# Optimization experiments

Hardware: AMD Instinct MI355X
Metric: run time of the kernel (lower is better)

The kernel has to match this reference:

```python
import jax, jax.numpy as jnp
import numpy as np
import math

B, L, D = 4, 2048, 512
H = 8
HD = D // H
K1 = 64  # local_window_size
K2 = 64  # global_window_size


def semi_local_mask(seq_len):
    # Faithful to create_semi_local_mask: anti-diagonal band + global prefix, ANDed with causal tril.
    i = jnp.arange(seq_len)[:, None]
    j = jnp.arange(seq_len)[None, :]
    band = (i + j >= seq_len - K1) & (i + j <= seq_len)
    glob = (j <= K2) & (j <= seq_len - i)
    causal = j <= i
    return (band | glob) & causal  # [L, L] bool


def setup_inputs() -> dict:
    key = jax.random.key(0)
    ks = jax.random.split(key, 8)
    def xavier(k, shape):
        fan_in, fan_out = shape[1], shape[0]
        lim = math.sqrt(6.0 / (fan_in + fan_out))
        return jax.random.uniform(k, shape, jnp.float32, -lim, lim)
    x = jax.random.normal(ks[0], (B, L, D), jnp.float32)
    w_qkv = xavier(ks[1], (3 * D, D)); b_qkv = jnp.zeros((3 * D,), jnp.float32)
    w_u = xavier(ks[2], (D, D));       b_u = jnp.zeros((D,), jnp.float32)
    w_out = xavier(ks[3], (D, D));     b_out = jnp.zeros((D,), jnp.float32)
    return {"x": x, "w_qkv": w_qkv, "b_qkv": b_qkv, "w_u": w_u, "b_u": b_u,
            "w_out": w_out, "b_out": b_out}


def reference(x, w_qkv, b_qkv, w_u, b_u, w_out, b_out):
    Bsz, Lq, Dm = x.shape
    qkv = (x @ w_qkv.T + b_qkv).reshape(Bsz, Lq, 3, H, HD)
    q, k, v = jnp.moveaxis(qkv, 2, 0)            # each [B, L, H, HD]
    q = jnp.transpose(q, (0, 2, 1, 3))           # [B, H, L, HD]
    k = jnp.transpose(k, (0, 2, 1, 3))
    v = jnp.transpose(v, (0, 2, 1, 3))
    u = x @ w_u.T + b_u                          # [B, L, D] (gate values)
    scale = 1.0 / math.sqrt(HD)
    scores = jnp.einsum('bhqd,bhkd->bhqk', q * scale, k)
    mask = semi_local_mask(Lq)                   # [L, L]
    scores = jnp.where(mask[None, None], scores, -jnp.inf)
    attn = jax.nn.softmax(scores, axis=-1)
    out = jnp.einsum('bhqk,bhkd->bhqd', attn, v)
    out = jnp.transpose(out, (0, 2, 1, 3)).reshape(Bsz, Lq, Dm)
    out = jax.nn.silu(out) * u
    return out @ w_out.T + b_out
```

## Files before the change

### kernel.cpp

```cpp
#include <hip/hip_runtime.h>
#include <hip/hip_bf16.h>

typedef __bf16 bf16x8 __attribute__((ext_vector_type(8)));
typedef float f32x4 __attribute__((ext_vector_type(4)));

#define B_ 4
#define L_ 2048
#define D_ 512
#define H_ 8

__device__ __forceinline__ void gl16(const __bf16* g, __bf16* l) {
  __builtin_amdgcn_global_load_lds(
      (const __attribute__((address_space(1))) void*)g,
      (__attribute__((address_space(3))) void*)l, 16, 0, 0);
}

__global__ __launch_bounds__(256) void cvt_pack(
    const float* __restrict__ x, const float* __restrict__ wq,
    const float* __restrict__ wu, const float* __restrict__ wo,
    const float* __restrict__ bq, const float* __restrict__ bu,
    __bf16* __restrict__ xb, __bf16* __restrict__ wcat,
    __bf16* __restrict__ wob, float* __restrict__ bcat)
{
  const int idx8 = blockIdx.x * 256 + threadIdx.x;
  const float* src; __bf16* dst; size_t so, dof;
  if (idx8 < 524288)      { src = x;  dst = xb;   so = (size_t)idx8 * 8;            dof = so; }
  else if (idx8 < 622592) { src = wq; dst = wcat; so = (size_t)(idx8 - 524288) * 8; dof = so; }
  else if (idx8 < 655360) { src = wu; dst = wcat; so = (size_t)(idx8 - 622592) * 8; dof = so + 786432; }
  else                    { src = wo; dst = wob;  so = (size_t)(idx8 - 655360) * 8; dof = so; }
  const float4 lo = *(const float4*)(src + so);
  const float4 hi = *(const float4*)(src + so + 4);
  bf16x8 r;
  r[0] = (__bf16)lo.x; r[1] = (__bf16)lo.y; r[2] = (__bf16)lo.z; r[3] = (__bf16)lo.w;
  r[4] = (__bf16)hi.x; r[5] = (__bf16)hi.y; r[6] = (__bf16)hi.z; r[7] = (__bf16)hi.w;
  *(bf16x8*)(dst + dof) = r;
  if (blockIdx.x == 0) {
#pragma unroll
    for (int e = 0; e < 8; ++e) {
      const int col = threadIdx.x * 8 + e;
      bcat[col] = (col < 1536) ? bq[col] : bu[col - 1536];
    }
  }
}

__global__ __launch_bounds__(512, 2) void gemm256(
    const __bf16* __restrict__ A, const __bf16* __restrict__ W,
    const float* __restrict__ bias, __bf16* __restrict__ C,
    int M, int N, int K)
{
  extern __shared__ char smem[];
  const int t = threadIdx.x;
  const int lane = t & 63;
  const int wave = t >> 6;
  const int wm = (wave >> 2) * 128;
  const int wn = (wave & 3) * 64;
  const int bm0 = blockIdx.x * 256;
  const int bn0 = blockIdx.y * 256;
  const int r = lane & 15, q = lane >> 4;
  const int nt = K >> 6;

  auto stage = [&](int kt, int p) {
#pragma unroll
    for (int j = 0; j < 4; ++j) {
      const int c = t + j * 512;
      const int row = c >> 3;
      const int cs = (c & 7) ^ (row & 7);
      gl16(A + (size_t)(bm0 + row) * K + kt * 64 + cs * 8,
           (__bf16*)(smem + p * 32768) + c * 8);
    }
#pragma unroll
    for (int j = 0; j < 4; ++j) {
      const int c = t + j * 512;
      const int row = c >> 3;
      const int cs = (c & 7) ^ (row & 7);
      gl16(W + (size_t)(bn0 + row) * K + kt * 64 + cs * 8,
           (__bf16*)(smem + 65536 + p * 32768) + c * 8);
    }
  };
  auto rdA = [&](int p, int mi, int ks) -> bf16x8 {
    const int row = wm + mi * 16 + r;
    const int byte = row * 128 + ((ks * 64 + q * 16) ^ ((row & 7) << 4));
    return *(const bf16x8*)(smem + p * 32768 + byte);
  };
  auto rdB = [&](int p, int ni, int ks) -> bf16x8 {
    const int row = wn + ni * 16 + r;
    const int byte = row * 128 + ((ks * 64 + q * 16) ^ ((row & 7) << 4));
    return *(const bf16x8*)(smem + 65536 + p * 32768 + byte);
  };

  f32x4 acc[8][4] = {};

  stage(0, 0);
  stage(1, 1);

  for (int kt = 0; kt < nt; ++kt) {
    const int p = kt & 1;
    if (kt < nt - 1) asm volatile("s_waitcnt vmcnt(8)" ::: "memory");
    else             asm volatile("s_waitcnt vmcnt(0)" ::: "memory");
    __builtin_amdgcn_sched_barrier(0);
    __builtin_amdgcn_s_barrier();
    __builtin_amdgcn_sched_barrier(0);

    bf16x8 a03[4][2], a47[4][2], b01[2][2], b23[2][2];
#pragma unroll
    for (int mi = 0; mi < 4; ++mi) { a03[mi][0] = rdA(p, mi, 0); a03[mi][1] = rdA(p, mi, 1); }
#pragma unroll
    for (int ni = 0; ni < 2; ++ni) { b01[ni][0] = rdB(p, ni, 0); b01[ni][1] = rdB(p, ni, 1); }
    __builtin_amdgcn_s_setprio(1);
#pragma unroll
    for (int mi = 0; mi < 4; ++mi)
#pragma unroll
      for (int ni = 0; ni < 2; ++ni) {
        acc[mi][ni] = __builtin_amdgcn_mfma_f32_16x16x32_bf16(a03[mi][0], b01[ni][0], acc[mi][ni], 0, 0, 0);
        acc[mi][ni] = __builtin_amdgcn_mfma_f32_16x16x32_bf16(a03[mi][1], b01[ni][1], acc[mi][ni], 0, 0, 0);
      }
    __builtin_amdgcn_s_setprio(0);
#pragma unroll
    for (int ni = 0; ni < 2; ++ni) { b23[ni][0] = rdB(p, ni + 2, 0); b23[ni][1] = rdB(p, ni + 2, 1); }
    __builtin_amdgcn_s_setprio(1);
#pragma unroll
    for (int mi = 0; mi < 4; ++mi)
#pragma unroll
      for (int ni = 0; ni < 2; ++ni) {
        acc[mi][ni + 2] = __builtin_amdgcn_mfma_f32_16x16x32_bf16(a03[mi][0], b23[ni][0], acc[mi][ni + 2], 0, 0, 0);
        acc[mi][ni + 2] = __builtin_amdgcn_mfma_f32_16x16x32_bf16(a03[mi][1], b23[ni][1], acc[mi][ni + 2], 0, 0, 0);
      }
    __builtin_amdgcn_s_setprio(0);
#pragma unroll
    for (int mi = 0; mi < 4; ++mi) { a47[mi][0] = rdA(p, mi + 4, 0); a47[mi][1] = rdA(p, mi + 4, 1); }
    __builtin_amdgcn_s_setprio(1);
#pragma unroll
    for (int mi = 0; mi < 4; ++mi)
#pragma unroll
      for (int ni = 0; ni < 2; ++ni) {
        acc[mi + 4][ni] = __builtin_amdgcn_mfma_f32_16x16x32_bf16(a47[mi][0], b01[ni][0], acc[mi + 4][ni], 0, 0, 0);
        acc[mi + 4][ni] = __builtin_amdgcn_mfma_f32_16x16x32_bf16(a47[mi][1], b01[ni][1], acc[mi + 4][ni], 0, 0, 0);
      }
    __builtin_amdgcn_s_setprio(0);
    asm volatile("s_waitcnt lgkmcnt(0)" ::: "memory");
    __builtin_amdgcn_sched_barrier(0);
    __builtin_amdgcn_s_barrier();
    __builtin_amdgcn_sched_barrier(0);
    if (kt + 2 < nt) stage(kt + 2, p);
    __builtin_amdgcn_s_setprio(1);
#pragma unroll
    for (int mi = 0; mi < 4; ++mi)
#pragma unroll
      for (int ni = 0; ni < 2; ++ni) {
        acc[mi + 4][ni + 2] = __builtin_amdgcn_mfma_f32_16x16x32_bf16(a47[mi][0], b23[ni][0], acc[mi + 4][ni + 2], 0, 0, 0);
        acc[mi + 4][ni + 2] = __builtin_amdgcn_mfma_f32_16x16x32_bf16(a47[mi][1], b23[ni][1], acc[mi + 4][ni + 2], 0, 0, 0);
      }
    __builtin_amdgcn_s_setprio(0);
  }

  const int cc = lane & 15, cq = lane >> 4;
#pragma unroll
  for (int mi = 0; mi < 8; ++mi) {
#pragma unroll
    for (int ni = 0; ni < 4; ++ni) {
      const int gcol = bn0 + wn + ni * 16 + cc;
      const float bv = bias[gcol];
#pragma unroll
      for (int rr = 0; rr < 4; ++rr) {
        const int grow = bm0 + wm + mi * 16 + cq * 4 + rr;
        C[(size_t)grow * N + gcol] = (__bf16)(acc[mi][ni][rr] + bv);
      }
    }
  }
}

template <typename TOUT>
__global__ __launch_bounds__(256) void gemm_async(
    const __bf16* __restrict__ A, const __bf16* __restrict__ W,
    const float* __restrict__ bias, TOUT* __restrict__ C,
    int M, int N, int K)
{
  __shared__ __bf16 lA[4096];
  __shared__ __bf16 lB[4096];
  const int t = threadIdx.x;
  const int lane = t & 63;
  const int wave = t >> 6;
  const int bm0 = blockIdx.x * 128;
  const int bn0 = blockIdx.y * 128;
  const int wm = (wave >> 1) * 64;
  const int wn = (wave & 1) * 64;

  f32x4 acc[4][4] = {};

  const __bf16* Ap0 = A + (size_t)(bm0 + (t >> 2)) * K + (t & 3) * 8;
  const __bf16* Bp0 = W + (size_t)(bn0 + (t >> 2)) * K + (t & 3) * 8;
  const size_t r64 = (size_t)64 * K;

  for (int k0 = 0; k0 < K; k0 += 32) {
    __syncthreads();
    gl16(Ap0 + k0,       lA + t * 8);
    gl16(Ap0 + r64 + k0, lA + (t + 256) * 8);
    gl16(Bp0 + k0,       lB + t * 8);
    gl16(Bp0 + r64 + k0, lB + (t + 256) * 8);
    __syncthreads();

    const int r = lane & 15, q = lane >> 4;
    bf16x8 af[4], bfr[4];
#pragma unroll
    for (int mi = 0; mi < 4; ++mi) af[mi] = ((const bf16x8*)lA)[(wm + mi * 16 + r) * 4 + q];
#pragma unroll
    for (int ni = 0; ni < 4; ++ni) bfr[ni] = ((const bf16x8*)lB)[(wn + ni * 16 + r) * 4 + q];
#pragma unroll
    for (int mi = 0; mi < 4; ++mi)
#pragma unroll
      for (int ni = 0; ni < 4; ++ni)
        acc[mi][ni] = __builtin_amdgcn_mfma_f32_16x16x32_bf16(af[mi], bfr[ni], acc[mi][ni], 0, 0, 0);
  }

  const int cc = lane & 15, cq = lane >> 4;
#pragma unroll
  for (int mi = 0; mi < 4; ++mi) {
#pragma unroll
    for (int ni = 0; ni < 4; ++ni) {
      const int gcol = bn0 + wn + ni * 16 + cc;
      const float bv = bias[gcol];
#pragma unroll
      for (int rr = 0; rr < 4; ++rr) {
        const int grow = bm0 + wm + mi * 16 + cq * 4 + rr;
        C[(size_t)grow * N + gcol] = (TOUT)(acc[mi][ni][rr] + bv);
      }
    }
  }
}

#define SP 72
#define QS 2048
__global__ __launch_bounds__(256) void attn_tile(
    const __bf16* __restrict__ qu,
    __bf16* __restrict__ g)
{
  const int qt = blockIdx.x, h = blockIdx.y, b = blockIdx.z;
  const int t = threadIdx.x;
  const int lane = t & 63;
  const int w = t >> 6;
  const int q0 = qt * 64, qmax = q0 + 63;
  const size_t bL = (size_t)b * L_;

  __shared__ __bf16 lK[4096];
  __shared__ __bf16 lV[64 * SP];
  __shared__ __bf16 Pb[64 * SP];

  const int cq = lane >> 4, cc = lane & 15;

  bf16x8 aq0, aq1;
  {
    const __bf16* qsrc = qu + (bL + q0 + w * 16 + cc) * QS + h * 64 + cq * 8;
    aq0 = *(const bf16x8*)qsrc;
    aq1 = *(const bf16x8*)(qsrc + 32);
  }

  float mreg[4], lreg[4];
#pragma unroll
  for (int rr = 0; rr < 4; ++rr) { mreg[rr] = -1e30f; lreg[rr] = 0.f; }
  f32x4 acc_o[4] = {};

  int clist[5]; int ncl = 0;
  clist[ncl++] = 0;
  if (qmax >= 64) clist[ncl++] = 64;
  {
    int lo = 1921 - q0; if (lo < 0) lo = 0; lo &= ~63;
    const int hik = min(qmax, 2048 - q0);
    for (int c = lo; c <= hik; c += 64)
      if (c >= 128) clist[ncl++] = c;
  }

  for (int ci = 0; ci < ncl; ++ci) {
    const int c0 = clist[ci];
    __syncthreads();
    {
      const int row = t >> 2, gb = t & 3;
      const __bf16* src = qu + (bL + c0 + row) * QS + 512 + h * 64;
      bf16x8 k0 = *(const bf16x8*)(src + gb * 8);
      bf16x8 k1 = *(const bf16x8*)(src + gb * 8 + 32);
      char* lkb = (char*)lK;
      const int sw = (row & 7) << 4;
      *(bf16x8*)(lkb + ((row * 128 + gb * 16) ^ sw))      = k0;
      *(bf16x8*)(lkb + ((row * 128 + gb * 16 + 64) ^ sw)) = k1;
    }
    {
      const int key = lane;
      const __bf16* src = qu + (bL + c0 + key) * QS + 1024 + h * 64 + w * 16;
      bf16x8 va = *(const bf16x8*)src;
      bf16x8 vb = *(const bf16x8*)(src + 8);
#pragma unroll
      for (int e = 0; e < 8; ++e) {
        lV[(w * 16 + e) * SP + key]     = va[e];
        lV[(w * 16 + 8 + e) * SP + key] = vb[e];
      }
    }
    __syncthreads();

    f32x4 s[4];
    {
      const char* lkb = (const char*)lK;
#pragma unroll
      for (int nt = 0; nt < 4; ++nt) {
        const int krow = nt * 16 + cc;
        const int sw = (krow & 7) << 4;
        bf16x8 bk0 = *(const bf16x8*)(lkb + ((krow * 128 + cq * 16) ^ sw));
        bf16x8 bk1 = *(const bf16x8*)(lkb + ((krow * 128 + 64 + cq * 16) ^ sw));
        f32x4 a = {};
        a = __builtin_amdgcn_mfma_f32_16x16x32_bf16(aq0, bk0, a, 0, 0, 0);
        a = __builtin_amdgcn_mfma_f32_16x16x32_bf16(aq1, bk1, a, 0, 0, 0);
        s[nt] = a;
      }
    }

#pragma unroll
    for (int nt = 0; nt < 4; ++nt) {
#pragma unroll
      for (int rr = 0; rr < 4; ++rr) {
        const int i = q0 + w * 16 + cq * 4 + rr;
        const int j = c0 + nt * 16 + cc;
        const int ij = i + j;
        const bool valid = (j <= i) &&
            ((ij >= 1984 && ij <= 2048) || (j <= 64 && ij <= 2048));
        s[nt][rr] = valid ? s[nt][rr] * 0.125f : -1e30f;
      }
    }

    f32x4 pm;
#pragma unroll
    for (int rr = 0; rr < 4; ++rr)
      pm[rr] = fmaxf(fmaxf(s[0][rr], s[1][rr]), fmaxf(s[2][rr], s[3][rr]));
#pragma unroll
    for (int m = 1; m < 16; m <<= 1) {
#pragma unroll
      for (int rr = 0; rr < 4; ++rr)
        pm[rr] = fmaxf(pm[rr], __shfl_xor(pm[rr], m, 64));
    }
    float corr[4];
#pragma unroll
    for (int rr = 0; rr < 4; ++rr) {
      const float nm = fmaxf(mreg[rr], pm[rr]);
      corr[rr] = __expf(mreg[rr] - nm);
      mreg[rr] = nm;
    }

    f32x4 ps = {};
#pragma unroll
    for (int nt = 0; nt < 4; ++nt) {
#pragma unroll
      for (int rr = 0; rr < 4; ++rr) {
        const float p = __expf(s[nt][rr] - mreg[rr]);
        ps[rr] += p;
        Pb[(w * 16 + cq * 4 + rr) * SP + nt * 16 + cc] = (__bf16)p;
      }
    }
#pragma unroll
    for (int m = 1; m < 16; m <<= 1) {
#pragma unroll
      for (int rr = 0; rr < 4; ++rr)
        ps[rr] += __shfl_xor(ps[rr], m, 64);
    }
#pragma unroll
    for (int rr = 0; rr < 4; ++rr) lreg[rr] = lreg[rr] * corr[rr] + ps[rr];

    {
      bf16x8 pa0 = *(const bf16x8*)(Pb + (w * 16 + cc) * SP + cq * 8);
      bf16x8 pa1 = *(const bf16x8*)(Pb + (w * 16 + cc) * SP + 32 + cq * 8);
#pragma unroll
      for (int dt = 0; dt < 4; ++dt) {
#pragma unroll
        for (int rr = 0; rr < 4; ++rr) acc_o[dt][rr] *= corr[rr];
        bf16x8 vb0 = *(const bf16x8*)(lV + (dt * 16 + cc) * SP + cq * 8);
        bf16x8 vb1 = *(const bf16x8*)(lV + (dt * 16 + cc) * SP + 32 + cq * 8);
        acc_o[dt] = __builtin_amdgcn_mfma_f32_16x16x32_bf16(pa0, vb0, acc_o[dt], 0, 0, 0);
        acc_o[dt] = __builtin_amdgcn_mfma_f32_16x16x32_bf16(pa1, vb1, acc_o[dt], 0, 0, 0);
      }
    }
  }

#pragma unroll
  for (int dt = 0; dt < 4; ++dt) {
#pragma unroll
    for (int rr = 0; rr < 4; ++rr) {
      const int row16 = cq * 4 + rr;
      const size_t qrow = bL + q0 + w * 16 + row16;
      const int d = dt * 16 + cc;
      const float o = acc_o[dt][rr] / fmaxf(lreg[rr], 1e-30f);
      const float uv = (float)qu[qrow * QS + 1536 + h * 64 + d];
      g[qrow * D_ + h * 64 + d] = (__bf16)(o / (1.f + __expf(-o)) * uv);
    }
  }
}

extern "C" void kernel_launch(void* const* d_in, const int* in_sizes, int n_in,
                              void* d_out, int out_size, void* d_ws, size_t ws_size,
                              hipStream_t stream) {
  const float* x     = (const float*)d_in[0];
  const float* w_qkv = (const float*)d_in[1];
  const float* b_qkv = (const float*)d_in[2];
  const float* w_u   = (const float*)d_in[3];
  const float* b_u   = (const float*)d_in[4];
  const float* w_out = (const float*)d_in[5];
  const float* b_out = (const float*)d_in[6];
  float* out = (float*)d_out;

  char* ws = (char*)d_ws;
  __bf16* xb   = (__bf16*)ws;
  __bf16* wcat = (__bf16*)(ws + 8388608);
  __bf16* wob  = (__bf16*)(ws + 10485760);
  float*  bcat = (float*) (ws + 11010048);
  __bf16* qu   = (__bf16*)(ws + 11018240);
  __bf16* gb   = (__bf16*)(ws + 44572672);

  static bool attr_done = []() {
    hipFuncSetAttribute((const void*)gemm256,
                        hipFuncAttributeMaxDynamicSharedMemorySize, 131072);
    return true;
  }();
  (void)attr_done;

  cvt_pack<<<dim3(2688), dim3(256), 0, stream>>>(
      x, w_qkv, w_u, w_out, b_qkv, b_u, xb, wcat, wob, bcat);
  gemm256<<<dim3(32, 8), dim3(512), 131072, stream>>>(
      xb, wcat, bcat, qu, 8192, 2048, 512);
  attn_tile<<<dim3(L_ / 64, H_, B_), dim3(256), 0, stream>>>(qu, gb);
  gemm_async<float><<<dim3(64, 4), dim3(256), 0, stream>>>(
      gb, wob, b_out, out, 8192, 512, 512);
}
```

Baseline: 148.5 us.

## Add fine-grained barriers to GEMM loop and prefetch K/V in attention

In the GEMM main loop, extra workgroup barriers and lgkmcnt waits now sit between each LDS-read phase and its MFMA phase, so waves move through read and compute phases together. In the attention kernel, the K/V chunk for the next iteration is loaded from global memory into registers while the current chunk is being processed, replacing the synchronous load-then-store pattern. The first part adds several barriers per k-tile, which can cost stalls. The prefetch adds register pressure but hides global load latency.

```diff
diff --git a/kernel.cpp b/kernel.cpp
--- a/kernel.cpp
+++ b/kernel.cpp
@@ -88,6 +88,9 @@
     return *(const bf16x8*)(smem + 65536 + p * 32768 + byte);
   };
 
+#define SB0 __builtin_amdgcn_sched_barrier(0)
+#define LGKM0 asm volatile("s_waitcnt lgkmcnt(0)" ::: "memory")
+
   f32x4 acc[8][4] = {};
 
   stage(0, 0);
@@ -97,15 +100,16 @@
     const int p = kt & 1;
     if (kt < nt - 1) asm volatile("s_waitcnt vmcnt(8)" ::: "memory");
     else             asm volatile("s_waitcnt vmcnt(0)" ::: "memory");
-    __builtin_amdgcn_sched_barrier(0);
+    SB0;
     __builtin_amdgcn_s_barrier();
-    __builtin_amdgcn_sched_barrier(0);
+    SB0;
 
     bf16x8 a03[4][2], a47[4][2], b01[2][2], b23[2][2];
 #pragma unroll
     for (int mi = 0; mi < 4; ++mi) { a03[mi][0] = rdA(p, mi, 0); a03[mi][1] = rdA(p, mi, 1); }
 #pragma unroll
     for (int ni = 0; ni < 2; ++ni) { b01[ni][0] = rdB(p, ni, 0); b01[ni][1] = rdB(p, ni, 1); }
+    SB0; __builtin_amdgcn_s_barrier(); LGKM0; SB0;
     __builtin_amdgcn_s_setprio(1);
 #pragma unroll
     for (int mi = 0; mi < 4; ++mi)
@@ -115,8 +119,10 @@
         acc[mi][ni] = __builtin_amdgcn_mfma_f32_16x16x32_bf16(a03[mi][1], b01[ni][1], acc[mi][ni], 0, 0, 0);
       }
     __builtin_amdgcn_s_setprio(0);
+    SB0; __builtin_amdgcn_s_barrier(); SB0;
 #pragma unroll
     for (int ni = 0; ni < 2; ++ni) { b23[ni][0] = rdB(p, ni + 2, 0); b23[ni][1] = rdB(p, ni + 2, 1); }
+    SB0; __builtin_amdgcn_s_barrier(); LGKM0; SB0;
     __builtin_amdgcn_s_setprio(1);
 #pragma unroll
     for (int mi = 0; mi < 4; ++mi)
@@ -126,8 +132,10 @@
         acc[mi][ni + 2] = __builtin_amdgcn_mfma_f32_16x16x32_bf16(a03[mi][1], b23[ni][1], acc[mi][ni + 2], 0, 0, 0);
       }
     __builtin_amdgcn_s_setprio(0);
+    SB0; __builtin_amdgcn_s_barrier(); SB0;
 #pragma unroll
     for (int mi = 0; mi < 4; ++mi) { a47[mi][0] = rdA(p, mi + 4, 0); a47[mi][1] = rdA(p, mi + 4, 1); }
+    SB0; __builtin_amdgcn_s_barrier(); LGKM0; SB0;
     __builtin_amdgcn_s_setprio(1);
 #pragma unroll
     for (int mi = 0; mi < 4; ++mi)
@@ -137,10 +145,7 @@
         acc[mi + 4][ni] = __builtin_amdgcn_mfma_f32_16x16x32_bf16(a47[mi][1], b01[ni][1], acc[mi + 4][ni], 0, 0, 0);
       }
     __builtin_amdgcn_s_setprio(0);
-    asm volatile("s_waitcnt lgkmcnt(0)" ::: "memory");
-    __builtin_amdgcn_sched_barrier(0);
-    __builtin_amdgcn_s_barrier();
-    __builtin_amdgcn_sched_barrier(0);
+    SB0; __builtin_amdgcn_s_barrier(); SB0;
     if (kt + 2 < nt) stage(kt + 2, p);
     __builtin_amdgcn_s_setprio(1);
 #pragma unroll
@@ -246,6 +251,7 @@
   __shared__ __bf16 Pb[64 * SP];
 
   const int cq = lane >> 4, cc = lane & 15;
+  const int krow_st = t >> 2, kgb = t & 3;
 
   bf16x8 aq0, aq1;
   {
@@ -269,31 +275,46 @@
       if (c >= 128) clist[ncl++] = c;
   }
 
+  bf16x8 k0r, k1r, var, vbr;
+  {
+    const __bf16* src = qu + (bL + clist[0] + krow_st) * QS + 512 + h * 64;
+    k0r = *(const bf16x8*)(src + kgb * 8);
+    k1r = *(const bf16x8*)(src + kgb * 8 + 32);
+    const __bf16* vsrc = qu + (bL + clist[0] + lane) * QS + 1024 + h * 64 + w * 16;
+    var = *(const bf16x8*)vsrc;
+    vbr = *(const bf16x8*)(vsrc + 8);
+  }
+
   for (int ci = 0; ci < ncl; ++ci) {
     const int c0 = clist[ci];
-    __syncthreads();
+    asm volatile("s_waitcnt vmcnt(0)" ::: "memory");
+    __builtin_amdgcn_sched_barrier(0);
+    __builtin_amdgcn_s_barrier();
+    __builtin_amdgcn_sched_barrier(0);
     {
-      const int row = t >> 2, gb = t & 3;
-      const __bf16* src = qu + (bL + c0 + row) * QS + 512 + h * 64;
-      bf16x8 k0 = *(const bf16x8*)(src + gb * 8);
-      bf16x8 k1 = *(const bf16x8*)(src + gb * 8 + 32);
       char* lkb = (char*)lK;
-      const int sw = (row & 7) << 4;
-      *(bf16x8*)(lkb + ((row * 128 + gb * 16) ^ sw))      = k0;
-      *(bf16x8*)(lkb + ((row * 128 + gb * 16 + 64) ^ sw)) = k1;
-    }
-    {
-      const int key = lane;
-      const __bf16* src = qu + (bL + c0 + key) * QS + 1024 + h * 64 + w * 16;
-      bf16x8 va = *(const bf16x8*)src;
-      bf16x8 vb = *(const bf16x8*)(src + 8);
+      const int sw = (krow_st & 7) << 4;
+      *(bf16x8*)(lkb + ((krow_st * 128 + kgb * 16) ^ sw))      = k0r;
+      *(bf16x8*)(lkb + ((krow_st * 128 + kgb * 16 + 64) ^ sw)) = k1r;
 #pragma unroll
       for (int e = 0; e < 8; ++e) {
-        lV[(w * 16 + e) * SP + key]     = va[e];
-        lV[(w * 16 + 8 + e) * SP + key] = vb[e];
-      }
-    }
-    __syncthreads();
+        lV[(w * 16 + e) * SP + lane]     = var[e];
+        lV[(w * 16 + 8 + e) * SP + lane] = vbr[e];
+      }
+    }
+    if (ci + 1 < ncl) {
+      const int cn = clist[ci + 1];
+      const __bf16* src = qu + (bL + cn + krow_st) * QS + 512 + h * 64;
+      k0r = *(const bf16x8*)(src + kgb * 8);
+      k1r = *(const bf16x8*)(src + kgb * 8 + 32);
+      const __bf16* vsrc = qu + (bL + cn + lane) * QS + 1024 + h * 64 + w * 16;
+      var = *(const bf16x8*)(vsrc);
+      vbr = *(const bf16x8*)(vsrc + 8);
+    }
+    asm volatile("s_waitcnt lgkmcnt(0)" ::: "memory");
+    __builtin_amdgcn_sched_barrier(0);
+    __builtin_amdgcn_s_barrier();
+    __builtin_amdgcn_sched_barrier(0);
 
     f32x4 s[4];
     {
```

New measurement: 148.3 us. Within noise of the previous version (-0.1%).
